# Optimization experiments

Hardware: AMD Instinct MI355X
Metric: run time of the kernel (lower is better)

## Reference

```python
import jax, jax.numpy as jnp
import numpy as np

NUM_EMBEDDINGS = 1024
EMBEDDING_DIM = 64
SCALE = 1.0 / NUM_EMBEDDINGS


def setup_inputs() -> dict:
    key = jax.random.key(0)
    k1, k2 = jax.random.split(key)
    input = jax.random.normal(k1, (16, EMBEDDING_DIM, 64, 64), dtype=jnp.float32)
    # nn.Embedding weight initialized uniform(-scale, scale)
    codebook = jax.random.uniform(k2, (NUM_EMBEDDINGS, EMBEDDING_DIM),
                                  dtype=jnp.float32, minval=-SCALE, maxval=SCALE)
    return {"input": input, "codebook": codebook}


def reference(input, codebook):
    # NCHW -> NHWC, flatten spatial+batch to tokens [N, D]
    x = jnp.transpose(input, (0, 2, 3, 1))           # [B, H, W, D]
    B, H, W, D = x.shape
    flat = x.reshape(-1, D)                          # [N, D]
    dists = (jnp.sum(flat ** 2, axis=1, keepdims=True)
             + jnp.sum(codebook ** 2, axis=1)
             - 2.0 * flat @ codebook.T)              # [N, K]
    idx = jnp.argmin(dists, axis=-1).reshape(B, H, W)  # [B, H, W]
    quantized = codebook[idx]                        # [B, H, W, D]
    return jnp.transpose(quantized, (0, 3, 1, 2))    # [B, D, H, W]
```

## Files before the change

kernel.cpp:

```cpp
#include <hip/hip_runtime.h>

typedef short short8 __attribute__((ext_vector_type(8)));
typedef float f32x4 __attribute__((ext_vector_type(4)));
typedef unsigned long long u64;

#define NE 1024
#define D 64
#define HW 4096
#define NTOK 65536
#define MARGIN 3.0e-3f
#define FLT_MAX_F 3.402823466e+38f

#define WS_BN  0
#define WS_EBF 4096

__device__ __forceinline__ unsigned short f2bf(float f) {
    unsigned u = __float_as_uint(f);
    return (unsigned short)((u + 0x7fffu + ((u >> 16) & 1u)) >> 16);
}

__device__ __forceinline__ float np_sum64_sq(const float* v) {
    float s[8];
#pragma unroll
    for (int j = 0; j < 8; ++j) s[j] = __fmul_rn(v[j], v[j]);
#pragma unroll
    for (int i = 8; i < 64; i += 8) {
#pragma unroll
        for (int j = 0; j < 8; ++j)
            s[j] = __fadd_rn(s[j], __fmul_rn(v[i + j], v[i + j]));
    }
    return __fadd_rn(__fadd_rn(__fadd_rn(s[0], s[1]), __fadd_rn(s[2], s[3])),
                     __fadd_rn(__fadd_rn(s[4], s[5]), __fadd_rn(s[6], s[7])));
}

__global__ __launch_bounds__(256) void kP_prep(
        const float* __restrict__ cb, float* __restrict__ bn,
        unsigned short* __restrict__ ebf) {
    const int gid = blockIdx.x * 256 + threadIdx.x;
    ebf[gid] = f2bf(cb[gid]);
    if (gid < NE) {
        float row[D];
        const float4* r4 = reinterpret_cast<const float4*>(cb + (size_t)gid * D);
#pragma unroll
        for (int i = 0; i < 16; ++i) {
            float4 v = r4[i];
            row[4*i+0] = v.x; row[4*i+1] = v.y; row[4*i+2] = v.z; row[4*i+3] = v.w;
        }
        bn[gid] = np_sum64_sq(row);
    }
}

__global__ __launch_bounds__(256, 2) void k_mega(
        const float* __restrict__ in, const unsigned short* __restrict__ ebf,
        const float* __restrict__ bn_g, const float* __restrict__ cb,
        float* __restrict__ out) {
    __shared__ unsigned short ebq[128 * 64];
    __shared__ float sbn[NE];
    __shared__ u64 lmask[128 * 16];
    __shared__ unsigned short win_s[128];

    const int tid  = threadIdx.x;
    const int lane = tid & 63, w = tid >> 6;
    const int lcol = lane & 15, lhi = lane >> 4, lrow = lhi * 4;
    const int tokw = blockIdx.x * 128 + w * 32;
    const int b = tokw >> 12, hwb = tokw & 4095;

    {
        int4* mz = (int4*)lmask;
#pragma unroll
        for (int i = 0; i < 4; ++i) mz[tid + i * 256] = int4{0, 0, 0, 0};
    }
#pragma unroll
    for (int i = 0; i < 4; ++i) sbn[tid + i * 256] = bn_g[tid + i * 256];

    const float* xbase = in + (size_t)b * (D * HW);
    const int hw0 = hwb + lcol, hw1 = hw0 + 16;
    const int kb = lhi * 8;
    short8 B00, B01, B10, B11;
    {
        const float* p;
        p = xbase + (size_t)kb * HW + hw0;
#pragma unroll
        for (int j = 0; j < 8; ++j) B00[j] = (short)f2bf(p[(size_t)j * HW]);
        p = xbase + (size_t)(kb + 32) * HW + hw0;
#pragma unroll
        for (int j = 0; j < 8; ++j) B01[j] = (short)f2bf(p[(size_t)j * HW]);
        p = xbase + (size_t)kb * HW + hw1;
#pragma unroll
        for (int j = 0; j < 8; ++j) B10[j] = (short)f2bf(p[(size_t)j * HW]);
        p = xbase + (size_t)(kb + 32) * HW + hw1;
#pragma unroll
        for (int j = 0; j < 8; ++j) B11[j] = (short)f2bf(p[(size_t)j * HW]);
    }

    const int swz   = (lcol & 7) << 4;
    const int aoff0 = lcol * 128 + ((lhi * 16) ^ swz);
    const int aoff1 = lcol * 128 + ((64 + lhi * 16) ^ swz);

#define STAGE_CHUNK(C)                                                        \
    {                                                                         \
        const char* src = (const char*)(ebf + (size_t)(C) * 128 * 64);        \
        _Pragma("unroll")                                                     \
        for (int i = 0; i < 4; ++i) {                                         \
            int L = (tid + i * 256) * 16;                                     \
            int row = L >> 7, wi = L & 127;                                   \
            int4 v = *(const int4*)(src + L);                                 \
            *(int4*)((char*)ebq + row * 128 + (wi ^ ((row & 7) << 4))) = v;   \
        }                                                                     \
    }

#define CHUNK_MFMA(C, CT)                                                     \
    const char* lp = (const char*)ebq + (CT) * 2048;                          \
    short8 A0 = *(const short8*)(lp + aoff0);                                 \
    short8 A1 = *(const short8*)(lp + aoff1);                                 \
    f32x4 bnv = *(const f32x4*)(sbn + (C) * 128 + (CT) * 16 + lrow);          \
    f32x4 acc = {0.f, 0.f, 0.f, 0.f};                                         \
    acc = __builtin_amdgcn_mfma_f32_16x16x32_bf16(A0, B00, acc, 0, 0, 0);     \
    acc = __builtin_amdgcn_mfma_f32_16x16x32_bf16(A1, B01, acc, 0, 0, 0);     \
    f32x4 ac2 = {0.f, 0.f, 0.f, 0.f};                                         \
    ac2 = __builtin_amdgcn_mfma_f32_16x16x32_bf16(A0, B10, ac2, 0, 0, 0);     \
    ac2 = __builtin_amdgcn_mfma_f32_16x16x32_bf16(A1, B11, ac2, 0, 0, 0);

    float v10 = FLT_MAX_F, v11 = FLT_MAX_F;
    for (int c = 0; c < 8; ++c) {
        __syncthreads();
        STAGE_CHUNK(c)
        __syncthreads();
#pragma unroll
        for (int ct = 0; ct < 8; ++ct) {
            CHUNK_MFMA(c, ct)
#pragma unroll
            for (int r = 0; r < 4; ++r) {
                v10 = fminf(v10, __fmaf_rn(-2.0f, acc[r], bnv[r]));
                v11 = fminf(v11, __fmaf_rn(-2.0f, ac2[r], bnv[r]));
            }
        }
    }
    v10 = fminf(v10, __shfl_xor(v10, 16)); v10 = fminf(v10, __shfl_xor(v10, 32));
    v11 = fminf(v11, __shfl_xor(v11, 16)); v11 = fminf(v11, __shfl_xor(v11, 32));
    const float thr0 = v10 + MARGIN, thr1 = v11 + MARGIN;
    const int tA = w * 32 + lcol, tB = tA + 16;

    for (int c = 0; c < 8; ++c) {
        __syncthreads();
        STAGE_CHUNK(c)
        __syncthreads();
#pragma unroll
        for (int ct = 0; ct < 8; ++ct) {
            CHUNK_MFMA(c, ct)
            const int kg = c * 128 + ct * 16 + lrow;
#pragma unroll
            for (int r = 0; r < 4; ++r) {
                float t0 = __fmaf_rn(-2.0f, acc[r], bnv[r]);
                if (t0 <= thr0)
                    atomicOr(&lmask[tA * 16 + ((kg + r) >> 6)], 1ull << ((kg + r) & 63));
                float t1 = __fmaf_rn(-2.0f, ac2[r], bnv[r]);
                if (t1 <= thr1)
                    atomicOr(&lmask[tB * 16 + ((kg + r) >> 6)], 1ull << ((kg + r) & 63));
            }
        }
    }
    __syncthreads();

    {
        const int tok_l = tid >> 1, sub = tid & 1;
        const int tok = blockIdx.x * 128 + tok_l;
        const int tb = tok >> 12, thw = tok & 4095;
        const float* x = in + (size_t)tb * (D * HW) + thw;
        float xv[D];
#pragma unroll
        for (int d = 0; d < D; ++d) xv[d] = x[(size_t)d * HW];
        const float a = np_sum64_sq(xv);

        u64 best = ~0ull;
        int kp = -1;
        int pos = 0;
        for (int wd = 0; wd < 16; ++wd) {
            u64 m = lmask[tok_l * 16 + wd];
            while (m) {
                const int k = wd * 64 + (int)__builtin_ctzll(m);
                m &= m - 1;
                if (((pos++) & 1) != sub) continue;
                if (kp < 0) { kp = k; continue; }
                const float* e0 = cb + (size_t)kp * D;
                const float* e1 = cb + (size_t)k * D;
                float d0 = 0.f, d1 = 0.f;
#pragma unroll
                for (int d = 0; d < 64; ++d) {
                    d0 = __fmaf_rn(xv[d], e0[d], d0);
                    d1 = __fmaf_rn(xv[d], e1[d], d1);
                }
                float q0 = __fsub_rn(__fadd_rn(a, bn_g[kp]), __fmul_rn(2.0f, d0));
                float q1 = __fsub_rn(__fadd_rn(a, bn_g[k]),  __fmul_rn(2.0f, d1));
                u64 key0 = (((u64)__float_as_uint(q0)) << 32) | (unsigned)kp;
                u64 key1 = (((u64)__float_as_uint(q1)) << 32) | (unsigned)k;
                u64 kmin = key0 < key1 ? key0 : key1;
                best = best < kmin ? best : kmin;
                kp = -1;
            }
        }
        if (kp >= 0) {
            const float* e0 = cb + (size_t)kp * D;
            float d0 = 0.f;
#pragma unroll
            for (int d = 0; d < 64; ++d) d0 = __fmaf_rn(xv[d], e0[d], d0);
            float q0 = __fsub_rn(__fadd_rn(a, bn_g[kp]), __fmul_rn(2.0f, d0));
            u64 key0 = (((u64)__float_as_uint(q0)) << 32) | (unsigned)kp;
            best = best < key0 ? best : key0;
        }
        {
            u64 v = __shfl_xor(best, 1);
            best = best < v ? best : v;
        }
        if (sub == 0) win_s[tok_l] = (unsigned short)(best & 0x3FFull);
    }
    __syncthreads();

    {
        const int tok_l = tid >> 1, half = tid & 1;
        const int tok = blockIdx.x * 128 + tok_l;
        const int gb = tok >> 12, ghw = tok & 4095;
        const unsigned k = win_s[tok_l];
        const float4* er = reinterpret_cast<const float4*>(cb + (size_t)k * D + half * 32);
        float* ot = out + (size_t)gb * (D * HW) + ghw;
#pragma unroll
        for (int i = 0; i < 8; ++i) {
            float4 e = er[i];
            ot[(size_t)(half * 32 + 4*i + 0) * HW] = e.x;
            ot[(size_t)(half * 32 + 4*i + 1) * HW] = e.y;
            ot[(size_t)(half * 32 + 4*i + 2) * HW] = e.z;
            ot[(size_t)(half * 32 + 4*i + 3) * HW] = e.w;
        }
    }
}

extern "C" void kernel_launch(void* const* d_in, const int* in_sizes, int n_in,
                              void* d_out, int out_size, void* d_ws, size_t ws_size,
                              hipStream_t stream) {
    const float* in  = (const float*)d_in[0];
    const float* cb  = (const float*)d_in[1];
    float*       out = (float*)d_out;
    char*        ws  = (char*)d_ws;

    float*          bn  = (float*)(ws + WS_BN);
    unsigned short* ebf = (unsigned short*)(ws + WS_EBF);

    hipLaunchKernelGGL(kP_prep, dim3(256), dim3(256), 0, stream, cb, bn, ebf);
    hipLaunchKernelGGL(k_mega,  dim3(512), dim3(256), 0, stream, in, ebf, bn, cb, out);
}
```

Baseline: 90.29 us.

## Prefetch codebook chunks into registers and build candidate masks without LDS atomics

The codebook chunk for the next iteration is now loaded from global memory into registers while the current chunk is consumed by MFMA, which overlaps global latency with compute. The second pass builds its candidate bitmasks in registers, merges them across lanes with shuffles and writes each mask word once, replacing per-hit LDS 64-bit atomics and the upfront zeroing of the mask. The mask row stride is padded to 17 to avoid bank conflicts, and launch bounds now request 4 blocks per SM. The trade-off is more register pressure under the higher occupancy bound, which may cause spills.

```diff
diff --git a/kernel.cpp b/kernel.cpp
--- a/kernel.cpp
+++ b/kernel.cpp
@@ -7,9 +7,9 @@
 #define NE 1024
 #define D 64
 #define HW 4096
-#define NTOK 65536
 #define MARGIN 3.0e-3f
 #define FLT_MAX_F 3.402823466e+38f
+#define MSTRIDE 17
 
 #define WS_BN  0
 #define WS_EBF 4096
@@ -50,13 +50,13 @@
     }
 }
 
-__global__ __launch_bounds__(256, 2) void k_mega(
+__global__ __launch_bounds__(256, 4) void k_mega(
         const float* __restrict__ in, const unsigned short* __restrict__ ebf,
         const float* __restrict__ bn_g, const float* __restrict__ cb,
         float* __restrict__ out) {
     __shared__ unsigned short ebq[128 * 64];
     __shared__ float sbn[NE];
-    __shared__ u64 lmask[128 * 16];
+    __shared__ u64 lmask[128 * MSTRIDE];
     __shared__ unsigned short win_s[128];
 
     const int tid  = threadIdx.x;
@@ -65,11 +65,6 @@
     const int tokw = blockIdx.x * 128 + w * 32;
     const int b = tokw >> 12, hwb = tokw & 4095;
 
-    {
-        int4* mz = (int4*)lmask;
-#pragma unroll
-        for (int i = 0; i < 4; ++i) mz[tid + i * 256] = int4{0, 0, 0, 0};
-    }
 #pragma unroll
     for (int i = 0; i < 4; ++i) sbn[tid + i * 256] = bn_g[tid + i * 256];
 
@@ -97,17 +92,17 @@
     const int aoff0 = lcol * 128 + ((lhi * 16) ^ swz);
     const int aoff1 = lcol * 128 + ((64 + lhi * 16) ^ swz);
 
-#define STAGE_CHUNK(C)                                                        \
-    {                                                                         \
-        const char* src = (const char*)(ebf + (size_t)(C) * 128 * 64);        \
-        _Pragma("unroll")                                                     \
-        for (int i = 0; i < 4; ++i) {                                         \
-            int L = (tid + i * 256) * 16;                                     \
-            int row = L >> 7, wi = L & 127;                                   \
-            int4 v = *(const int4*)(src + L);                                 \
-            *(int4*)((char*)ebq + row * 128 + (wi ^ ((row & 7) << 4))) = v;   \
-        }                                                                     \
-    }
+    int4 pf0, pf1, pf2, pf3;
+#define LOADC(C) { const int4* s_ = (const int4*)(ebf + (size_t)(C) * 8192);  \
+                   pf0 = s_[tid]; pf1 = s_[tid + 256];                        \
+                   pf2 = s_[tid + 512]; pf3 = s_[tid + 768]; }
+#define WRITEC() { int4 t_[4] = {pf0, pf1, pf2, pf3};                         \
+    _Pragma("unroll")                                                         \
+    for (int i = 0; i < 4; ++i) {                                             \
+        int L = (tid + i * 256) * 16;                                         \
+        int row = L >> 7, wi = L & 127;                                       \
+        *(int4*)((char*)ebq + row * 128 + (wi ^ ((row & 7) << 4))) = t_[i];   \
+    } }
 
 #define CHUNK_MFMA(C, CT)                                                     \
     const char* lp = (const char*)ebq + (CT) * 2048;                          \
@@ -122,10 +117,12 @@
     ac2 = __builtin_amdgcn_mfma_f32_16x16x32_bf16(A1, B11, ac2, 0, 0, 0);
 
     float v10 = FLT_MAX_F, v11 = FLT_MAX_F;
+    LOADC(0)
     for (int c = 0; c < 8; ++c) {
         __syncthreads();
-        STAGE_CHUNK(c)
-        __syncthreads();
+        WRITEC()
+        __syncthreads();
+        LOADC(c < 7 ? c + 1 : 0)
 #pragma unroll
         for (int ct = 0; ct < 8; ++ct) {
             CHUNK_MFMA(c, ct)
@@ -143,21 +140,31 @@
 
     for (int c = 0; c < 8; ++c) {
         __syncthreads();
-        STAGE_CHUNK(c)
-        __syncthreads();
+        WRITEC()
+        __syncthreads();
+        if (c < 7) LOADC(c + 1)
+        u64 w0a = 0, w1a = 0, w0b = 0, w1b = 0;
 #pragma unroll
         for (int ct = 0; ct < 8; ++ct) {
             CHUNK_MFMA(c, ct)
-            const int kg = c * 128 + ct * 16 + lrow;
 #pragma unroll
             for (int r = 0; r < 4; ++r) {
+                const int bit = (ct & 3) * 16 + lrow + r;
                 float t0 = __fmaf_rn(-2.0f, acc[r], bnv[r]);
-                if (t0 <= thr0)
-                    atomicOr(&lmask[tA * 16 + ((kg + r) >> 6)], 1ull << ((kg + r) & 63));
+                if (t0 <= thr0) { if (ct < 4) w0a |= 1ull << bit; else w1a |= 1ull << bit; }
                 float t1 = __fmaf_rn(-2.0f, ac2[r], bnv[r]);
-                if (t1 <= thr1)
-                    atomicOr(&lmask[tB * 16 + ((kg + r) >> 6)], 1ull << ((kg + r) & 63));
+                if (t1 <= thr1) { if (ct < 4) w0b |= 1ull << bit; else w1b |= 1ull << bit; }
             }
+        }
+        w0a |= __shfl_xor(w0a, 16); w0a |= __shfl_xor(w0a, 32);
+        w1a |= __shfl_xor(w1a, 16); w1a |= __shfl_xor(w1a, 32);
+        w0b |= __shfl_xor(w0b, 16); w0b |= __shfl_xor(w0b, 32);
+        w1b |= __shfl_xor(w1b, 16); w1b |= __shfl_xor(w1b, 32);
+        if (lhi == 0) {
+            lmask[tA * MSTRIDE + 2 * c]     = w0a;
+            lmask[tA * MSTRIDE + 2 * c + 1] = w1a;
+            lmask[tB * MSTRIDE + 2 * c]     = w0b;
+            lmask[tB * MSTRIDE + 2 * c + 1] = w1b;
         }
     }
     __syncthreads();
@@ -176,7 +183,7 @@
         int kp = -1;
         int pos = 0;
         for (int wd = 0; wd < 16; ++wd) {
-            u64 m = lmask[tok_l * 16 + wd];
+            u64 m = lmask[tok_l * MSTRIDE + wd];
             while (m) {
                 const int k = wd * 64 + (int)__builtin_ctzll(m);
                 m &= m - 1;
```

Result: faster. 76.21 us (-15.6%).
